# Optimization experiments

Measured on AMD Instinct MI355X. Metric: run time of the kernel, lower is better.

## Reference

```python
import jax, jax.numpy as jnp
import numpy as np

N, NPER, B, E = 65536, 1024, 64, 1048576
IN_F, HID, K, NCLS = 128, 64, 16, 10


def setup_inputs() -> dict:
    key = jax.random.key(0)
    ks = jax.random.split(key, 12)
    x = jax.random.normal(ks[0], (N, IN_F), jnp.float32)
    # block-structured intra-graph edges: 64 graphs of 1024 contiguous nodes
    gid = jax.random.randint(ks[1], (E,), 0, B)
    src = gid * NPER + jax.random.randint(ks[2], (E,), 0, NPER)
    dst = gid * NPER + jax.random.randint(ks[3], (E,), 0, NPER)
    edge_index = jnp.stack([src, dst]).astype(jnp.int32)
    batch = (jnp.arange(N, dtype=jnp.int32) // NPER).astype(jnp.int32)
    def lin(k, fo, fi):
        kw, kb = jax.random.split(k)
        s = 1.0 / np.sqrt(fi)
        return (jax.random.uniform(kw, (fo, fi), jnp.float32, -s, s),
                jax.random.uniform(kb, (fo,), jnp.float32, -s, s))
    W1, b1 = lin(ks[4], HID, IN_F)
    W2, b2 = lin(ks[5], HID, HID)
    Wp, bp = lin(ks[6], K, HID)      # DMoN cluster-assignment MLP (single Linear)
    Wl, bl = lin(ks[7], NCLS, HID)   # final classifier
    return {"x": x, "edge_index": edge_index, "batch": batch,
            "W1": W1, "b1": b1, "W2": W2, "b2": b2,
            "Wp": Wp, "bp": bp, "Wl": Wl, "bl": bl}


def gcn_conv(x, src, dst, W, b):
    # GCNConv with add_self_loops=True, symmetric normalization
    n = x.shape[0]
    deg = jax.ops.segment_sum(jnp.ones(src.shape[0], x.dtype), dst,
                              num_segments=n) + 1.0  # +1 for self-loop
    dinv = jax.lax.rsqrt(deg)
    h = x @ W.T
    coef = (dinv[src] * dinv[dst])[:, None]
    agg = jax.ops.segment_sum(h[src] * coef, dst, num_segments=n)
    agg = agg + h * (dinv * dinv)[:, None]  # self-loop contribution
    return agg + b


def reference(x, edge_index, batch, W1, b1, W2, b2, Wp, bp, Wl, bl):
    src, dst = edge_index[0], edge_index[1]
    h = jax.nn.relu(gcn_conv(x, src, dst, W1, b1))
    h = jax.nn.relu(gcn_conv(h, src, dst, W2, b2))
    # to_dense_batch: graphs are equal-sized and contiguous -> reshape, mask all True
    Xb = h.reshape(B, NPER, HID)
    # DMoN cluster assignment (dropout=0.0, mask all ones)
    s = jax.nn.softmax(Xb @ Wp.T + bp, axis=-1)          # [B, NPER, K]
    Xp = jax.nn.selu(jnp.einsum('bnk,bnh->bkh', s, Xb))   # pooled clusters [B, K, HID]
    out = Xp.mean(axis=1)                                  # [B, HID]
    logits = out @ Wl.T + bl                               # [B, NCLS]
    return logits
```

## Files before the change

kernel.cpp:

```cpp
#include <hip/hip_runtime.h>
#include <cstddef>

#define N_NODES 65536
#define NPER    1024
#define NGRAPH  64
#define HID     64
#define IN_F    128
#define KCLUS   16
#define NCLS    10
#define ECAP    20480
#define HSTRIDE 12
#define ZROW    NPER
#define LIN_BLOCKS 1024

template <int K>
__device__ __forceinline__ void gemm_tile64(const float* __restrict__ X,
                                            const float* __restrict__ W,
                                            float* __restrict__ Y,
                                            float (*xs)[68], float (*ws)[68],
                                            int block, int t) {
    const size_t row0 = (size_t)block * 64;
    const int rbase = t >> 3;
    const int cbase = t & 7;
    float acc[2][8] = {};

    for (int kc = 0; kc < K; kc += 64) {
        __syncthreads();
        for (int i = t; i < 64 * 16; i += 256) {
            int row = i >> 4, k4 = (i & 15) << 2;
            *(float4*)&xs[row][k4] = *(const float4*)(X + (row0 + row) * K + kc + k4);
        }
        for (int i = t; i < 64 * 16; i += 256) {
            int col = i >> 4, k4 = (i & 15) << 2;
            *(float4*)&ws[col][k4] = *(const float4*)(W + col * K + kc + k4);
        }
        __syncthreads();

#pragma unroll 4
        for (int k4 = 0; k4 < 64; k4 += 4) {
            float4 xr[2], wr[8];
#pragma unroll
            for (int rr = 0; rr < 2; ++rr) xr[rr] = *(const float4*)&xs[rbase + 32 * rr][k4];
#pragma unroll
            for (int cc = 0; cc < 8; ++cc) wr[cc] = *(const float4*)&ws[cbase + 8 * cc][k4];
#pragma unroll
            for (int rr = 0; rr < 2; ++rr)
#pragma unroll
                for (int cc = 0; cc < 8; ++cc) {
                    acc[rr][cc] = fmaf(xr[rr].x, wr[cc].x, acc[rr][cc]);
                    acc[rr][cc] = fmaf(xr[rr].y, wr[cc].y, acc[rr][cc]);
                    acc[rr][cc] = fmaf(xr[rr].z, wr[cc].z, acc[rr][cc]);
                    acc[rr][cc] = fmaf(xr[rr].w, wr[cc].w, acc[rr][cc]);
                }
        }
    }

#pragma unroll
    for (int rr = 0; rr < 2; ++rr)
#pragma unroll
        for (int cc = 0; cc < 8; ++cc)
            Y[(row0 + rbase + 32 * rr) * HID + cbase + 8 * cc] = acc[rr][cc];
}

template <int K>
__device__ __forceinline__ void gemm_tile(const float* __restrict__ X,
                                          const float* __restrict__ W,
                                          float* __restrict__ Y,
                                          float (*xs)[68], float (*ws)[68],
                                          int block, int t) {
    const size_t row0 = (size_t)block * 128;
    const int rbase = t >> 3;
    const int cbase = t & 7;
    float acc[4][8] = {};

    for (int kc = 0; kc < K; kc += 64) {
        __syncthreads();
        for (int i = t; i < 128 * 16; i += 256) {
            int row = i >> 4, k4 = (i & 15) << 2;
            *(float4*)&xs[row][k4] = *(const float4*)(X + (row0 + row) * K + kc + k4);
        }
        for (int i = t; i < 64 * 16; i += 256) {
            int col = i >> 4, k4 = (i & 15) << 2;
            *(float4*)&ws[col][k4] = *(const float4*)(W + col * K + kc + k4);
        }
        __syncthreads();

#pragma unroll 4
        for (int k4 = 0; k4 < 64; k4 += 4) {
            float4 xr[4], wr[8];
#pragma unroll
            for (int rr = 0; rr < 4; ++rr) xr[rr] = *(const float4*)&xs[rbase + 32 * rr][k4];
#pragma unroll
            for (int cc = 0; cc < 8; ++cc) wr[cc] = *(const float4*)&ws[cbase + 8 * cc][k4];
#pragma unroll
            for (int rr = 0; rr < 4; ++rr)
#pragma unroll
                for (int cc = 0; cc < 8; ++cc) {
                    acc[rr][cc] = fmaf(xr[rr].x, wr[cc].x, acc[rr][cc]);
                    acc[rr][cc] = fmaf(xr[rr].y, wr[cc].y, acc[rr][cc]);
                    acc[rr][cc] = fmaf(xr[rr].z, wr[cc].z, acc[rr][cc]);
                    acc[rr][cc] = fmaf(xr[rr].w, wr[cc].w, acc[rr][cc]);
                }
        }
    }

#pragma unroll
    for (int rr = 0; rr < 4; ++rr)
#pragma unroll
        for (int cc = 0; cc < 8; ++cc)
            Y[(row0 + rbase + 32 * rr) * HID + cbase + 8 * cc] = acc[rr][cc];
}

__global__ __launch_bounds__(256) void front_kernel(const float* __restrict__ X,
                                                    const float* __restrict__ W,
                                                    float* __restrict__ Y,
                                                    const int* __restrict__ src,
                                                    const int* __restrict__ dst,
                                                    int* __restrict__ ecnt,
                                                    int* __restrict__ gedges, int E) {
    __shared__ float xs[64][68];
    __shared__ float ws[64][68];
    const int t = threadIdx.x;

    if (blockIdx.x >= LIN_BLOCKS) {
        int* hist = (int*)&xs[0][0];
        int* base_l = hist + NGRAPH;
        const int e0 = (blockIdx.x - LIN_BLOCKS) * 2048;
        if (t < NGRAPH) hist[t] = 0;
        __syncthreads();

        int gg[8], rr[8], pk[8];
#pragma unroll
        for (int i = 0; i < 8; ++i) {
            int idx = e0 + i * 256 + t;
            if (idx < E) {
                int d = dst[idx], s = src[idx];
                int g = d >> 10;
                gg[i] = g;
                pk[i] = ((d & 1023) << 10) | (s & 1023);
                rr[i] = atomicAdd(&hist[g], 1);
            } else gg[i] = -1;
        }
        __syncthreads();
        if (t < NGRAPH) base_l[t] = atomicAdd(&ecnt[t], hist[t]);
        __syncthreads();
#pragma unroll
        for (int i = 0; i < 8; ++i) {
            if (gg[i] >= 0) {
                int pos = base_l[gg[i]] + rr[i];
                if (pos < ECAP) gedges[gg[i] * ECAP + pos] = pk[i];
            }
        }
        return;
    }

    gemm_tile64<IN_F>(X, W, Y, xs, ws, blockIdx.x, t);
}

template <int K>
__global__ __launch_bounds__(256) void linear_kernel(const float* __restrict__ X,
                                                     const float* __restrict__ W,
                                                     float* __restrict__ Y) {
    __shared__ float xs[128][68];
    __shared__ float ws[64][68];
    gemm_tile<K>(X, W, Y, xs, ws, blockIdx.x, threadIdx.x);
}

__global__ __launch_bounds__(1024) void scatter_kernel(const int* __restrict__ gedges,
                                                       const int* __restrict__ ecnt,
                                                       int* __restrict__ rp,
                                                       unsigned short* __restrict__ esorted,
                                                       float* __restrict__ dinv) {
    __shared__ int hist[NPER];
    __shared__ int wsum[16];
    const int g = blockIdx.x >> 3;
    const int sub = blockIdx.x & 7;
    const int t = threadIdx.x;
    const int lane = t & 63, wid = t >> 6;
    const int ec = ecnt[g];
    const int* ge = gedges + (size_t)g * ECAP;

    hist[t] = 0;
    __syncthreads();
    for (int i = t; i < ec; i += 1024) atomicAdd(&hist[ge[i] >> 10], 1);
    __syncthreads();

    const int h0 = hist[t];
    const int pd = (h0 + 3) & ~3;
    int v = pd;
#pragma unroll
    for (int off = 1; off < 64; off <<= 1) {
        int x = __shfl_up(v, off, 64);
        if (lane >= off) v += x;
    }
    if (lane == 63) wsum[wid] = v;
    __syncthreads();
    if (wid == 0) {
        int wv = (lane < 16) ? wsum[lane] : 0;
#pragma unroll
        for (int off = 1; off < 16; off <<= 1) {
            int x = __shfl_up(wv, off, 64);
            if (lane >= off) wv += x;
        }
        if (lane < 16) wsum[lane] = wv;
    }
    __syncthreads();
    const int incl = v + (wid > 0 ? wsum[wid - 1] : 0);
    const int excl = incl - pd;

    if (sub == 0) {
        rp[g * (NPER + 1) + t] = excl;
        if (t == NPER - 1) rp[g * (NPER + 1) + NPER] = incl;
        dinv[g * NPER + t] = rsqrtf((float)h0 + 1.0f);
    }
    __syncthreads();
    hist[t] = excl;
    __syncthreads();

    unsigned short* es = esorted + (size_t)g * ECAP;

    if ((t >> 7) == sub)
        for (int q = excl + h0; q < excl + pd; ++q) es[q] = (unsigned short)ZROW;

    for (int i = t; i < ec; i += 1024) {
        int pk = ge[i];
        int d = pk >> 10;
        if ((d >> 7) == sub) {
            int pos = atomicAdd(&hist[d], 1);
            es[pos] = (unsigned short)(pk & 1023);
        }
    }
}

__global__ __launch_bounds__(512) void agg_kernel(const float* __restrict__ h,
                                                  const unsigned short* __restrict__ esorted,
                                                  const int* __restrict__ rp,
                                                  const float* __restrict__ dinv,
                                                  const float* __restrict__ bias,
                                                  float* __restrict__ outp) {
    __shared__ float Hs[(NPER + 1) * HSTRIDE];
    const int g = blockIdx.x & 63;
    const int f0 = (blockIdx.x >> 6) * 8;
    const int t = threadIdx.x;
    const int base = g * NPER;

    for (int r = t; r < NPER; r += 512) {
        const float* hp = h + (size_t)(base + r) * HID + f0;
        float4 a = *(const float4*)hp;
        float4 b = *(const float4*)(hp + 4);
        float dv = dinv[base + r];
        float* row = &Hs[r * HSTRIDE];
        *(float4*)row = make_float4(a.x * dv, a.y * dv, a.z * dv, a.w * dv);
        *(float4*)(row + 4) = make_float4(b.x * dv, b.y * dv, b.z * dv, b.w * dv);
    }
    if (t < HSTRIDE) Hs[ZROW * HSTRIDE + t] = 0.f;
    float bb[8];
#pragma unroll
    for (int j = 0; j < 8; ++j) bb[j] = bias[f0 + j];
    const unsigned short* es = esorted + (size_t)g * ECAP;
    const int* rpg = rp + g * (NPER + 1);
    __syncthreads();

    for (int ld = t; ld < NPER; ld += 512) {
        int p = rpg[ld];
        const int pe = rpg[ld + 1];
        const float* srow = &Hs[ld * HSTRIDE];
        float4 acc0 = *(const float4*)srow;
        float4 acc1 = *(const float4*)(srow + 4);
        float4 bcc0 = make_float4(0.f, 0.f, 0.f, 0.f);
        float4 bcc1 = make_float4(0.f, 0.f, 0.f, 0.f);

        for (; p < pe; p += 4) {
            uint2 w4 = *(const uint2*)(es + p);
            const float* r0 = &Hs[(int)(w4.x & 0xFFFFu) * HSTRIDE];
            const float* r1 = &Hs[(int)(w4.x >> 16) * HSTRIDE];
            const float* r2 = &Hs[(int)(w4.y & 0xFFFFu) * HSTRIDE];
            const float* r3 = &Hs[(int)(w4.y >> 16) * HSTRIDE];
            float4 a0 = *(const float4*)r0, a1 = *(const float4*)(r0 + 4);
            float4 b0 = *(const float4*)r1, b1 = *(const float4*)(r1 + 4);
            float4 c0v = *(const float4*)r2, c1v = *(const float4*)(r2 + 4);
            float4 d0 = *(const float4*)r3, d1 = *(const float4*)(r3 + 4);
            acc0.x += a0.x; acc0.y += a0.y; acc0.z += a0.z; acc0.w += a0.w;
            acc1.x += a1.x; acc1.y += a1.y; acc1.z += a1.z; acc1.w += a1.w;
            bcc0.x += b0.x; bcc0.y += b0.y; bcc0.z += b0.z; bcc0.w += b0.w;
            bcc1.x += b1.x; bcc1.y += b1.y; bcc1.z += b1.z; bcc1.w += b1.w;
            acc0.x += c0v.x; acc0.y += c0v.y; acc0.z += c0v.z; acc0.w += c0v.w;
            acc1.x += c1v.x; acc1.y += c1v.y; acc1.z += c1v.z; acc1.w += c1v.w;
            bcc0.x += d0.x; bcc0.y += d0.y; bcc0.z += d0.z; bcc0.w += d0.w;
            bcc1.x += d1.x; bcc1.y += d1.y; bcc1.z += d1.z; bcc1.w += d1.w;
        }
        acc0.x += bcc0.x; acc0.y += bcc0.y; acc0.z += bcc0.z; acc0.w += bcc0.w;
        acc1.x += bcc1.x; acc1.y += bcc1.y; acc1.z += bcc1.z; acc1.w += bcc1.w;

        const float dv = dinv[base + ld];
        float4 o0, o1;
        o0.x = fmaxf(fmaf(acc0.x, dv, bb[0]), 0.f);
        o0.y = fmaxf(fmaf(acc0.y, dv, bb[1]), 0.f);
        o0.z = fmaxf(fmaf(acc0.z, dv, bb[2]), 0.f);
        o0.w = fmaxf(fmaf(acc0.w, dv, bb[3]), 0.f);
        o1.x = fmaxf(fmaf(acc1.x, dv, bb[4]), 0.f);
        o1.y = fmaxf(fmaf(acc1.y, dv, bb[5]), 0.f);
        o1.z = fmaxf(fmaf(acc1.z, dv, bb[6]), 0.f);
        o1.w = fmaxf(fmaf(acc1.w, dv, bb[7]), 0.f);
        float* op = outp + (size_t)(base + ld) * HID + f0;
        *(float4*)op = o0;
        *(float4*)(op + 4) = o1;
    }
}

__global__ __launch_bounds__(256) void pool1_kernel(const float* __restrict__ h,
                                                    const float* __restrict__ Wp,
                                                    const float* __restrict__ bp,
                                                    float* __restrict__ xpart) {
    __shared__ float xs[128][HID + 1];
    __shared__ float ss[128][KCLUS + 1];
    __shared__ float wp[KCLUS][HID];
    __shared__ float bps[KCLUS];
    const int g = blockIdx.x >> 3;
    const int c = blockIdx.x & 7;
    const int t = threadIdx.x;
    const float* hb = h + ((size_t)g * NPER + c * 128) * HID;

    for (int i = t; i < 128 * HID / 4; i += 256) {
        float4 v = ((const float4*)hb)[i];
        int row = i >> 4, col = (i & 15) * 4;
        xs[row][col] = v.x; xs[row][col + 1] = v.y; xs[row][col + 2] = v.z; xs[row][col + 3] = v.w;
    }
    for (int i = t; i < KCLUS * HID; i += 256) wp[i >> 6][i & 63] = Wp[i];
    if (t < KCLUS) bps[t] = bp[t];
    __syncthreads();

    if (t < 128) {
        float lg[KCLUS];
        float mx = -1e30f;
#pragma unroll
        for (int k = 0; k < KCLUS; ++k) {
            float a = bps[k];
#pragma unroll 8
            for (int hh = 0; hh < HID; ++hh) a = fmaf(xs[t][hh], wp[k][hh], a);
            lg[k] = a;
            mx = fmaxf(mx, a);
        }
        float sum = 0.f;
#pragma unroll
        for (int k = 0; k < KCLUS; ++k) {
            lg[k] = __expf(lg[k] - mx);
            sum += lg[k];
        }
        float inv = 1.0f / sum;
#pragma unroll
        for (int k = 0; k < KCLUS; ++k) ss[t][k] = lg[k] * inv;
    }
    __syncthreads();

    const int hcol = t & 63;
    const int k0 = (t >> 6) * 4;
    float a0 = 0.f, a1 = 0.f, a2 = 0.f, a3 = 0.f;
#pragma unroll 8
    for (int n = 0; n < 128; ++n) {
        float xv = xs[n][hcol];
        a0 = fmaf(ss[n][k0 + 0], xv, a0);
        a1 = fmaf(ss[n][k0 + 1], xv, a1);
        a2 = fmaf(ss[n][k0 + 2], xv, a2);
        a3 = fmaf(ss[n][k0 + 3], xv, a3);
    }
    float* xp = xpart + (((size_t)(g * 8 + c)) * KCLUS + k0) * HID + hcol;
    xp[0] = a0; xp[HID] = a1; xp[2 * HID] = a2; xp[3 * HID] = a3;
}

__global__ __launch_bounds__(256) void pool2_kernel(const float* __restrict__ xpart,
                                                    const float* __restrict__ Wl,
                                                    const float* __restrict__ bl,
                                                    float* __restrict__ out) {
    __shared__ float xp[KCLUS][HID + 1];
    __shared__ float outm[HID];
    const int g = blockIdx.x;
    const int t = threadIdx.x;
    const int hcol = t & 63;
    const int k0 = (t >> 6) * 4;
    const float* base = xpart + (size_t)g * 8 * KCLUS * HID;

    float a[4] = {};
#pragma unroll
    for (int c = 0; c < 8; ++c)
#pragma unroll
        for (int j = 0; j < 4; ++j)
            a[j] += base[(c * KCLUS + k0 + j) * HID + hcol];

    const float sc = 1.0507009873554805f, al = 1.6732632423543772f;
#pragma unroll
    for (int j = 0; j < 4; ++j) {
        float v = a[j];
        xp[k0 + j][hcol] = v > 0.f ? sc * v : sc * al * (__expf(v) - 1.f);
    }
    __syncthreads();

    if (t < HID) {
        float m = 0.f;
#pragma unroll
        for (int k = 0; k < KCLUS; ++k) m += xp[k][t];
        outm[t] = m * (1.0f / KCLUS);
    }
    __syncthreads();

    if (t < NCLS) {
        float acc = bl[t];
#pragma unroll 8
        for (int hh = 0; hh < HID; ++hh) acc = fmaf(outm[hh], Wl[t * HID + hh], acc);
        out[g * NCLS + t] = acc;
    }
}

extern "C" void kernel_launch(void* const* d_in, const int* in_sizes, int n_in,
                              void* d_out, int out_size, void* d_ws, size_t ws_size,
                              hipStream_t stream) {
    const float* x  = (const float*)d_in[0];
    const int* eidx = (const int*)d_in[1];
    const float* W1 = (const float*)d_in[3];
    const float* b1 = (const float*)d_in[4];
    const float* W2 = (const float*)d_in[5];
    const float* b2 = (const float*)d_in[6];
    const float* Wp = (const float*)d_in[7];
    const float* bp = (const float*)d_in[8];
    const float* Wl = (const float*)d_in[9];
    const float* bl = (const float*)d_in[10];
    float* out = (float*)d_out;

    const int E = in_sizes[1] / 2;
    const int* src = eidx;
    const int* dst = eidx + E;

    char* w = (char*)d_ws;
    int*            ecnt    = (int*)w;            w += 256;
    int*            gedges  = (int*)w;            w += (size_t)NGRAPH * ECAP * 4;
    unsigned short* esorted = (unsigned short*)w; w += (size_t)NGRAPH * ECAP * 2;
    int*            rp      = (int*)w;            w += (size_t)NGRAPH * (NPER + 1) * 4;
    float*          dinv    = (float*)w;          w += (size_t)N_NODES * 4;
    float*          A       = (float*)w;          w += (size_t)N_NODES * HID * 4;
    float*          Bf      = (float*)w;          w += (size_t)N_NODES * HID * 4;
    float*          xpart   = (float*)w;          w += (size_t)NGRAPH * 8 * KCLUS * HID * 4;

    hipMemsetAsync(ecnt, 0, 256, stream);

    const int nbucket = (E + 2047) / 2048;
    front_kernel<<<LIN_BLOCKS + nbucket, 256, 0, stream>>>(x, W1, A, src, dst, ecnt, gedges, E);

    scatter_kernel<<<NGRAPH * 8, 1024, 0, stream>>>(gedges, ecnt, rp, esorted, dinv);

    agg_kernel<<<NGRAPH * 8, 512, 0, stream>>>(A, esorted, rp, dinv, b1, Bf);

    linear_kernel<HID><<<N_NODES / 128, 256, 0, stream>>>(Bf, W2, A);
    agg_kernel<<<NGRAPH * 8, 512, 0, stream>>>(A, esorted, rp, dinv, b2, Bf);

    pool1_kernel<<<NGRAPH * 8, 256, 0, stream>>>(Bf, Wp, bp, xpart);
    pool2_kernel<<<NGRAPH, 256, 0, stream>>>(xpart, Wl, bl, out);
}
```

Baseline: 216.3 us.

## Reorder second GCN layer to aggregate first and fuse W2 into pooling

Uses the linearity of graph aggregation to swap the order of the second GCN layer. The raw layer-1 activations are now aggregated with symmetric normalization only, and the W2 matmul, bias and ReLU are applied inside the pooling kernel. This removes the standalone linear kernel launch and one full read/write pass over the node feature matrix. In exchange, the pooling kernel does an extra per-block 128x64x64 scalar GEMM and uses much more shared memory, which may lower its occupancy.

```diff
diff --git a/kernel.cpp b/kernel.cpp
--- a/kernel.cpp
+++ b/kernel.cpp
@@ -62,55 +62,6 @@
             Y[(row0 + rbase + 32 * rr) * HID + cbase + 8 * cc] = acc[rr][cc];
 }
 
-template <int K>
-__device__ __forceinline__ void gemm_tile(const float* __restrict__ X,
-                                          const float* __restrict__ W,
-                                          float* __restrict__ Y,
-                                          float (*xs)[68], float (*ws)[68],
-                                          int block, int t) {
-    const size_t row0 = (size_t)block * 128;
-    const int rbase = t >> 3;
-    const int cbase = t & 7;
-    float acc[4][8] = {};
-
-    for (int kc = 0; kc < K; kc += 64) {
-        __syncthreads();
-        for (int i = t; i < 128 * 16; i += 256) {
-            int row = i >> 4, k4 = (i & 15) << 2;
-            *(float4*)&xs[row][k4] = *(const float4*)(X + (row0 + row) * K + kc + k4);
-        }
-        for (int i = t; i < 64 * 16; i += 256) {
-            int col = i >> 4, k4 = (i & 15) << 2;
-            *(float4*)&ws[col][k4] = *(const float4*)(W + col * K + kc + k4);
-        }
-        __syncthreads();
-
-#pragma unroll 4
-        for (int k4 = 0; k4 < 64; k4 += 4) {
-            float4 xr[4], wr[8];
-#pragma unroll
-            for (int rr = 0; rr < 4; ++rr) xr[rr] = *(const float4*)&xs[rbase + 32 * rr][k4];
-#pragma unroll
-            for (int cc = 0; cc < 8; ++cc) wr[cc] = *(const float4*)&ws[cbase + 8 * cc][k4];
-#pragma unroll
-            for (int rr = 0; rr < 4; ++rr)
-#pragma unroll
-                for (int cc = 0; cc < 8; ++cc) {
-                    acc[rr][cc] = fmaf(xr[rr].x, wr[cc].x, acc[rr][cc]);
-                    acc[rr][cc] = fmaf(xr[rr].y, wr[cc].y, acc[rr][cc]);
-                    acc[rr][cc] = fmaf(xr[rr].z, wr[cc].z, acc[rr][cc]);
-                    acc[rr][cc] = fmaf(xr[rr].w, wr[cc].w, acc[rr][cc]);
-                }
-        }
-    }
-
-#pragma unroll
-    for (int rr = 0; rr < 4; ++rr)
-#pragma unroll
-        for (int cc = 0; cc < 8; ++cc)
-            Y[(row0 + rbase + 32 * rr) * HID + cbase + 8 * cc] = acc[rr][cc];
-}
-
 __global__ __launch_bounds__(256) void front_kernel(const float* __restrict__ X,
                                                     const float* __restrict__ W,
                                                     float* __restrict__ Y,
@@ -155,15 +106,6 @@
     }
 
     gemm_tile64<IN_F>(X, W, Y, xs, ws, blockIdx.x, t);
-}
-
-template <int K>
-__global__ __launch_bounds__(256) void linear_kernel(const float* __restrict__ X,
-                                                     const float* __restrict__ W,
-                                                     float* __restrict__ Y) {
-    __shared__ float xs[128][68];
-    __shared__ float ws[64][68];
-    gemm_tile<K>(X, W, Y, xs, ws, blockIdx.x, threadIdx.x);
 }
 
 __global__ __launch_bounds__(1024) void scatter_kernel(const int* __restrict__ gedges,
@@ -232,6 +174,7 @@
     }
 }
 
+template <bool FIN>
 __global__ __launch_bounds__(512) void agg_kernel(const float* __restrict__ h,
                                                   const unsigned short* __restrict__ esorted,
                                                   const int* __restrict__ rp,
@@ -256,7 +199,7 @@
     if (t < HSTRIDE) Hs[ZROW * HSTRIDE + t] = 0.f;
     float bb[8];
 #pragma unroll
-    for (int j = 0; j < 8; ++j) bb[j] = bias[f0 + j];
+    for (int j = 0; j < 8; ++j) bb[j] = FIN ? bias[f0 + j] : 0.f;
     const unsigned short* es = esorted + (size_t)g * ECAP;
     const int* rpg = rp + g * (NPER + 1);
     __syncthreads();
@@ -294,40 +237,67 @@
 
         const float dv = dinv[base + ld];
         float4 o0, o1;
-        o0.x = fmaxf(fmaf(acc0.x, dv, bb[0]), 0.f);
-        o0.y = fmaxf(fmaf(acc0.y, dv, bb[1]), 0.f);
-        o0.z = fmaxf(fmaf(acc0.z, dv, bb[2]), 0.f);
-        o0.w = fmaxf(fmaf(acc0.w, dv, bb[3]), 0.f);
-        o1.x = fmaxf(fmaf(acc1.x, dv, bb[4]), 0.f);
-        o1.y = fmaxf(fmaf(acc1.y, dv, bb[5]), 0.f);
-        o1.z = fmaxf(fmaf(acc1.z, dv, bb[6]), 0.f);
-        o1.w = fmaxf(fmaf(acc1.w, dv, bb[7]), 0.f);
+        if (FIN) {
+            o0.x = fmaxf(fmaf(acc0.x, dv, bb[0]), 0.f);
+            o0.y = fmaxf(fmaf(acc0.y, dv, bb[1]), 0.f);
+            o0.z = fmaxf(fmaf(acc0.z, dv, bb[2]), 0.f);
+            o0.w = fmaxf(fmaf(acc0.w, dv, bb[3]), 0.f);
+            o1.x = fmaxf(fmaf(acc1.x, dv, bb[4]), 0.f);
+            o1.y = fmaxf(fmaf(acc1.y, dv, bb[5]), 0.f);
+            o1.z = fmaxf(fmaf(acc1.z, dv, bb[6]), 0.f);
+            o1.w = fmaxf(fmaf(acc1.w, dv, bb[7]), 0.f);
+        } else {
+            o0.x = acc0.x * dv; o0.y = acc0.y * dv; o0.z = acc0.z * dv; o0.w = acc0.w * dv;
+            o1.x = acc1.x * dv; o1.y = acc1.y * dv; o1.z = acc1.z * dv; o1.w = acc1.w * dv;
+        }
         float* op = outp + (size_t)(base + ld) * HID + f0;
         *(float4*)op = o0;
         *(float4*)(op + 4) = o1;
     }
 }
 
-__global__ __launch_bounds__(256) void pool1_kernel(const float* __restrict__ h,
-                                                    const float* __restrict__ Wp,
-                                                    const float* __restrict__ bp,
-                                                    float* __restrict__ xpart) {
+__global__ __launch_bounds__(256) void pool1f_kernel(const float* __restrict__ G,
+                                                     const float* __restrict__ W2,
+                                                     const float* __restrict__ b2,
+                                                     const float* __restrict__ Wp,
+                                                     const float* __restrict__ bp,
+                                                     float* __restrict__ xpart) {
     __shared__ float xs[128][HID + 1];
     __shared__ float ss[128][KCLUS + 1];
     __shared__ float wp[KCLUS][HID];
     __shared__ float bps[KCLUS];
+    __shared__ float w2s[HID][HID + 1];
+    __shared__ float b2s[HID];
     const int g = blockIdx.x >> 3;
     const int c = blockIdx.x & 7;
     const int t = threadIdx.x;
-    const float* hb = h + ((size_t)g * NPER + c * 128) * HID;
+    const float* hb = G + ((size_t)g * NPER + c * 128) * HID;
 
     for (int i = t; i < 128 * HID / 4; i += 256) {
         float4 v = ((const float4*)hb)[i];
         int row = i >> 4, col = (i & 15) * 4;
         xs[row][col] = v.x; xs[row][col + 1] = v.y; xs[row][col + 2] = v.z; xs[row][col + 3] = v.w;
     }
+    for (int i = t; i < HID * HID; i += 256) w2s[i >> 6][i & 63] = W2[i];
     for (int i = t; i < KCLUS * HID; i += 256) wp[i >> 6][i & 63] = Wp[i];
     if (t < KCLUS) bps[t] = bp[t];
+    if (t < HID) b2s[t] = b2[t];
+    __syncthreads();
+
+    {
+        const int row = t >> 1;
+        const int half = (t & 1) * 32;
+        float acc[32];
+#pragma unroll
+        for (int j = 0; j < 32; ++j) acc[j] = b2s[half + j];
+        for (int k = 0; k < HID; ++k) {
+            float gv = xs[row][k];
+#pragma unroll
+            for (int j = 0; j < 32; ++j) acc[j] = fmaf(gv, w2s[half + j][k], acc[j]);
+        }
+#pragma unroll
+        for (int j = 0; j < 32; ++j) xs[row][half + j] = fmaxf(acc[j], 0.f);
+    }
     __syncthreads();
 
     if (t < 128) {
@@ -447,11 +417,10 @@
 
     scatter_kernel<<<NGRAPH * 8, 1024, 0, stream>>>(gedges, ecnt, rp, esorted, dinv);
 
-    agg_kernel<<<NGRAPH * 8, 512, 0, stream>>>(A, esorted, rp, dinv, b1, Bf);
-
-    linear_kernel<HID><<<N_NODES / 128, 256, 0, stream>>>(Bf, W2, A);
-    agg_kernel<<<NGRAPH * 8, 512, 0, stream>>>(A, esorted, rp, dinv, b2, Bf);
-
-    pool1_kernel<<<NGRAPH * 8, 256, 0, stream>>>(Bf, Wp, bp, xpart);
+    agg_kernel<true><<<NGRAPH * 8, 512, 0, stream>>>(A, esorted, rp, dinv, b1, Bf);
+
+    agg_kernel<false><<<NGRAPH * 8, 512, 0, stream>>>(Bf, esorted, rp, dinv, b1, A);
+
+    pool1f_kernel<<<NGRAPH * 8, 256, 0, stream>>>(A, W2, b2, Wp, bp, xpart);
     pool2_kernel<<<NGRAPH, 256, 0, stream>>>(xpart, Wl, bl, out);
 }
```

Result: slower. 225.1 us (+4.1%).
